# Optimization experiments

Hardware: AMD Instinct MI355X
Metric: run time of the kernel (lower is better)

## Reference

```python
import jax, jax.numpy as jnp
import numpy as np

D_MODEL = 1024
N_HEAD = 16
DEPTH = D_MODEL // N_HEAD
B, N = 2, 2048


def setup_inputs() -> dict:
    key = jax.random.key(0)
    ks = jax.random.split(key, 9)
    s = 1.0 / np.sqrt(D_MODEL)
    inp = {
        "input": jax.random.normal(ks[0], (B, N, D_MODEL), dtype=jnp.float32),
        # causal boolean mask; True = keep (module masks where mask is False)
        "mask": jnp.broadcast_to(jnp.tril(jnp.ones((N, N), dtype=bool)), (B, N, N)),
        "Wq": jax.random.uniform(ks[1], (D_MODEL, D_MODEL), jnp.float32, -s, s),
        "bq": jax.random.uniform(ks[2], (D_MODEL,), jnp.float32, -s, s),
        "Wk": jax.random.uniform(ks[3], (D_MODEL, D_MODEL), jnp.float32, -s, s),
        "bk": jax.random.uniform(ks[4], (D_MODEL,), jnp.float32, -s, s),
        "Wv": jax.random.uniform(ks[5], (D_MODEL, D_MODEL), jnp.float32, -s, s),
        "bv": jax.random.uniform(ks[6], (D_MODEL,), jnp.float32, -s, s),
        "Wo": jax.random.uniform(ks[7], (D_MODEL, D_MODEL), jnp.float32, -s, s),
        "bo": jax.random.uniform(ks[8], (D_MODEL,), jnp.float32, -s, s),
    }
    return inp


def reference(input, mask, Wq, bq, Wk, bk, Wv, bv, Wo, bo):
    b, n, _ = input.shape
    # projections (dropout in eval mode = identity)
    q = (input @ Wq.T + bq).reshape(b, n, N_HEAD, DEPTH)
    k = (input @ Wk.T + bk).reshape(b, n, N_HEAD, DEPTH)
    v = (input @ Wv.T + bv).reshape(b, n, N_HEAD, DEPTH)
    scale = 1.0 / np.sqrt(DEPTH)
    # scores: [b, h, q, k]
    scores = jnp.einsum("bqhd,bkhd->bhqk", q, k) * scale
    scores = jnp.where(mask[:, None, :, :], scores, -jnp.inf)
    attn = jax.nn.softmax(scores, axis=-1)
    out = jnp.einsum("bhqk,bkhd->bqhd", attn, v).reshape(b, n, D_MODEL)
    return out @ Wo.T + bo
```

## Files before the change

kernel.cpp:

```cpp
#include <hip/hip_runtime.h>
#include <stdint.h>

#define DM 1024
#define NH 16
#define DEPTH 64
#define BB 2
#define NN 2048
#define ROWS (BB*NN)

typedef __attribute__((ext_vector_type(8))) short short8;
typedef __attribute__((ext_vector_type(4))) short short4v;
typedef __attribute__((ext_vector_type(4))) float f32x4;

static __device__ __forceinline__ unsigned short f2b(float f) {
  unsigned u = __float_as_uint(f);
  u += 0x7fffu + ((u >> 16) & 1u);
  return (unsigned short)(u >> 16);
}

__global__ void cvt5_kernel(const float* __restrict__ s0, const float* __restrict__ s1,
                            const float* __restrict__ s2, const float* __restrict__ s3,
                            const float* __restrict__ s4,
                            unsigned short* __restrict__ d0, unsigned short* __restrict__ d1,
                            unsigned short* __restrict__ d2, unsigned short* __restrict__ d3,
                            unsigned short* __restrict__ d4) {
  const float* src; unsigned short* dst; int n4;
  const int seg = blockIdx.y;
  if (seg == 0)      { src = s0; dst = d0; n4 = ROWS * DM / 4; }
  else if (seg == 1) { src = s1; dst = d1; n4 = DM * DM / 4; }
  else if (seg == 2) { src = s2; dst = d2; n4 = DM * DM / 4; }
  else if (seg == 3) { src = s3; dst = d3; n4 = DM * DM / 4; }
  else               { src = s4; dst = d4; n4 = DM * DM / 4; }
  int i = blockIdx.x * blockDim.x + threadIdx.x;
  int stride = gridDim.x * blockDim.x;
  for (; i < n4; i += stride) {
    float4 v = reinterpret_cast<const float4*>(src)[i];
    short4v o;
    o.x = (short)f2b(v.x); o.y = (short)f2b(v.y);
    o.z = (short)f2b(v.z); o.w = (short)f2b(v.w);
    reinterpret_cast<short4v*>(dst)[i] = o;
  }
}

template<int OUTF32>
__global__ __launch_bounds__(256)
void gemm_bt(const unsigned short* __restrict__ A, const unsigned short* __restrict__ B,
             const float* __restrict__ bias0, const float* __restrict__ bias1,
             const float* __restrict__ bias2, float sc0,
             float* __restrict__ Cf, unsigned short* __restrict__ Cb,
             int K, int N) {
  __shared__ unsigned short As[128 * 32];
  __shared__ unsigned short Bs[128 * 32];
  const int tid = threadIdx.x;
  const int lane = tid & 63;
  const int w = tid >> 6;
  const int wr = w >> 1, wc = w & 1;
  const int l15 = lane & 15, l4 = lane >> 4;
  const int m0 = blockIdx.y * 128, n0 = blockIdx.x * 128;
  f32x4 acc[4][4] = {};
  const int nkt = K >> 5;
  for (int kt = 0; kt < nkt; ++kt) {
    const int kbase = kt * 32;
#pragma unroll
    for (int i = 0; i < 2; ++i) {
      int c = tid + i * 256;
      int row = c >> 2, ko = (c & 3) * 8;
      __builtin_amdgcn_global_load_lds(
          (__attribute__((address_space(1))) void*)(A + (size_t)(m0 + row) * K + kbase + ko),
          (__attribute__((address_space(3))) void*)((char*)As + c * 16), 16, 0, 0);
      __builtin_amdgcn_global_load_lds(
          (__attribute__((address_space(1))) void*)(B + (size_t)(n0 + row) * K + kbase + ko),
          (__attribute__((address_space(3))) void*)((char*)Bs + c * 16), 16, 0, 0);
    }
    __syncthreads();
    short8 a[4], b[4];
#pragma unroll
    for (int mi = 0; mi < 4; ++mi)
      a[mi] = *reinterpret_cast<const short8*>(&As[(wr * 64 + mi * 16 + l15) * 32 + l4 * 8]);
#pragma unroll
    for (int ni = 0; ni < 4; ++ni)
      b[ni] = *reinterpret_cast<const short8*>(&Bs[(wc * 64 + ni * 16 + l15) * 32 + l4 * 8]);
#pragma unroll
    for (int mi = 0; mi < 4; ++mi)
#pragma unroll
      for (int ni = 0; ni < 4; ++ni)
        acc[mi][ni] = __builtin_amdgcn_mfma_f32_16x16x32_bf16(a[mi], b[ni], acc[mi][ni], 0, 0, 0);
    __syncthreads();
  }
  const float* bp = bias0; int boff = 0;
  if (n0 >= 2048)      { bp = bias2; boff = 2048; }
  else if (n0 >= 1024) { bp = bias1; boff = 1024; }
  const float sc = (n0 < 1024) ? sc0 : 1.0f;
#pragma unroll
  for (int ni = 0; ni < 4; ++ni) {
    int col = n0 + wc * 64 + ni * 16 + l15;
    float bv = bp[col - boff];
#pragma unroll
    for (int mi = 0; mi < 4; ++mi) {
      f32x4 v = acc[mi][ni];
#pragma unroll
      for (int r = 0; r < 4; ++r) {
        int row = m0 + wr * 64 + mi * 16 + l4 * 4 + r;
        float outv = (v[r] + bv) * sc;
        if (OUTF32) Cf[(size_t)row * N + col] = outv;
        else        Cb[(size_t)row * N + col] = f2b(outv);
      }
    }
  }
}

__global__ __launch_bounds__(256)
void vtrans_kernel(const unsigned short* __restrict__ qkv, unsigned short* __restrict__ vt) {
  const int bh = blockIdx.y, b = bh >> 4, h = bh & 15;
  const int n0 = blockIdx.x * 64;
  __shared__ unsigned short t[64][72];
  const unsigned short* src = qkv + (size_t)(b * NN) * 3072 + 2048 + h * 64;
#pragma unroll
  for (int i = 0; i < 2; ++i) {
    int c = threadIdx.x + i * 256;
    int row = c >> 3, d0 = (c & 7) * 8;
    short8 v = *reinterpret_cast<const short8*>(src + (size_t)(n0 + row) * 3072 + d0);
#pragma unroll
    for (int j = 0; j < 8; ++j) t[d0 + j][row] = (unsigned short)v[j];
  }
  __syncthreads();
  unsigned short* dst = vt + ((size_t)(b * NH + h) * DEPTH) * NN + n0;
#pragma unroll
  for (int i = 0; i < 2; ++i) {
    int c = threadIdx.x + i * 256;
    int d = c >> 3, nn0 = (c & 7) * 8;
    short8 v;
#pragma unroll
    for (int j = 0; j < 8; ++j) v[j] = (short)t[d][nn0 + j];
    *reinterpret_cast<short8*>(dst + (size_t)d * NN + nn0) = v;
  }
}

__global__ __launch_bounds__(256)
void attn_kernel(const unsigned short* __restrict__ qkv, const unsigned short* __restrict__ vt,
                 unsigned short* __restrict__ aout) {
  const int tid = threadIdx.x, lane = tid & 63, w = tid >> 6;
  const int l15 = lane & 15, l4 = lane >> 4;
  const unsigned u = blockIdx.x * 4 + w;
  const int bh = u >> 6;
  const int ii = u & 63;
  const int b = bh >> 4, h = bh & 15;
  const unsigned short* Qp  = qkv + (size_t)(b * NN) * 3072 + h * 64;
  const unsigned short* Kp  = Qp + 1024;
  const unsigned short* Vtp = vt + (size_t)(b * NH + h) * DEPTH * NN;
  __shared__ unsigned short plds[4][16 * 40];
  unsigned short* pw = plds[w];

  for (int ip = 0; ip < 2; ++ip) {
    const int qt = ip ? (127 - ii) : ii;
    const int qp0 = qt * 16;
    const int nkt = (qt >> 1) + 1;
    short8 qf[2];
#pragma unroll
    for (int kk = 0; kk < 2; ++kk)
      qf[kk] = *reinterpret_cast<const short8*>(
          Qp + (size_t)(qp0 + l15) * 3072 + kk * 32 + l4 * 8);
    f32x4 o[4] = {};
    float m = -3.0e38f, l = 0.0f;
    short8 kf[2][2];
#pragma unroll
    for (int cf = 0; cf < 2; ++cf)
#pragma unroll
      for (int kk = 0; kk < 2; ++kk)
        kf[cf][kk] = *reinterpret_cast<const short8*>(
            Kp + (size_t)(cf * 16 + l15) * 3072 + kk * 32 + l4 * 8);

    for (int kt = 0; kt < nkt; ++kt) {
      const int k0 = kt * 32;
      f32x4 s[2];
#pragma unroll
      for (int cf = 0; cf < 2; ++cf) {
        f32x4 z = {};
        z = __builtin_amdgcn_mfma_f32_16x16x32_bf16(kf[cf][0], qf[0], z, 0, 0, 0);
        s[cf] = __builtin_amdgcn_mfma_f32_16x16x32_bf16(kf[cf][1], qf[1], z, 0, 0, 0);
      }
      short8 vf[4];
#pragma unroll
      for (int dn = 0; dn < 4; ++dn)
        vf[dn] = *reinterpret_cast<const short8*>(
            Vtp + (size_t)(dn * 16 + l15) * NN + k0 + l4 * 8);
      const int kn = (kt + 1 < nkt) ? k0 + 32 : k0;
#pragma unroll
      for (int cf = 0; cf < 2; ++cf)
#pragma unroll
        for (int kk = 0; kk < 2; ++kk)
          kf[cf][kk] = *reinterpret_cast<const short8*>(
              Kp + (size_t)(kn + cf * 16 + l15) * 3072 + kk * 32 + l4 * 8);
      float p[2][4];
      const bool diag = (kt == nkt - 1);
#pragma unroll
      for (int cf = 0; cf < 2; ++cf)
#pragma unroll
        for (int r = 0; r < 4; ++r) {
          float x = s[cf][r];
          if (diag && (k0 + cf * 16 + l4 * 4 + r > qp0 + l15)) x = -3.0e38f;
          p[cf][r] = x;
        }
      float pm = fmaxf(
          fmaxf(fmaxf(p[0][0], p[0][1]), fmaxf(p[0][2], p[0][3])),
          fmaxf(fmaxf(p[1][0], p[1][1]), fmaxf(p[1][2], p[1][3])));
      pm = fmaxf(pm, __shfl_xor(pm, 16));
      pm = fmaxf(pm, __shfl_xor(pm, 32));
      const float mn = fmaxf(m, pm);
      const float al = __expf(m - mn);
      m = mn;
      float ps = 0.0f;
#pragma unroll
      for (int cf = 0; cf < 2; ++cf)
#pragma unroll
        for (int r = 0; r < 4; ++r) {
          p[cf][r] = __expf(p[cf][r] - mn);
          ps += p[cf][r];
        }
      ps += __shfl_xor(ps, 16);
      ps += __shfl_xor(ps, 32);
      l = l * al + ps;
#pragma unroll
      for (int cf = 0; cf < 2; ++cf)
#pragma unroll
        for (int hh = 0; hh < 2; ++hh) {
          unsigned pk;
          asm("v_cvt_pk_bf16_f32 %0, %1, %2"
              : "=v"(pk) : "v"(p[cf][2 * hh]), "v"(p[cf][2 * hh + 1]));
          *reinterpret_cast<unsigned*>(&pw[l15 * 40 + cf * 16 + l4 * 4 + 2 * hh]) = pk;
        }
#pragma unroll
      for (int dn = 0; dn < 4; ++dn)
#pragma unroll
        for (int r = 0; r < 4; ++r) o[dn][r] *= al;
      short8 pf = *reinterpret_cast<const short8*>(&pw[l15 * 40 + l4 * 8]);
#pragma unroll
      for (int dn = 0; dn < 4; ++dn)
        o[dn] = __builtin_amdgcn_mfma_f32_16x16x32_bf16(vf[dn], pf, o[dn], 0, 0, 0);
    }
    const float inv = 1.0f / l;
    const int row = b * NN + qp0 + l15;
#pragma unroll
    for (int dn = 0; dn < 4; ++dn) {
      short4v ov;
#pragma unroll
      for (int r = 0; r < 4; ++r) ov[r] = (short)f2b(o[dn][r] * inv);
      *reinterpret_cast<short4v*>(&aout[(size_t)row * DM + h * 64 + dn * 16 + l4 * 4]) = ov;
    }
  }
}

extern "C" void kernel_launch(void* const* d_in, const int* in_sizes, int n_in,
                              void* d_out, int out_size, void* d_ws, size_t ws_size,
                              hipStream_t stream) {
  const float* X  = (const float*)d_in[0];
  const float* Wq = (const float*)d_in[2];
  const float* bq = (const float*)d_in[3];
  const float* Wk = (const float*)d_in[4];
  const float* bk = (const float*)d_in[5];
  const float* Wv = (const float*)d_in[6];
  const float* bv = (const float*)d_in[7];
  const float* Wo = (const float*)d_in[8];
  const float* bo = (const float*)d_in[9];
  float* out = (float*)d_out;

  char* ws = (char*)d_ws;
  unsigned short* Xb     = (unsigned short*)(ws);
  unsigned short* Wstack = (unsigned short*)(ws + 8ull  * 1024 * 1024);
  unsigned short* Wob    = (unsigned short*)(ws + 14ull * 1024 * 1024);
  unsigned short* QKV    = (unsigned short*)(ws + 16ull * 1024 * 1024);
  unsigned short* Vt     = (unsigned short*)(ws + 40ull * 1024 * 1024);
  unsigned short* AOut   = (unsigned short*)(ws + 48ull * 1024 * 1024);

  cvt5_kernel<<<dim3(128, 5), 256, 0, stream>>>(X, Wq, Wk, Wv, Wo,
                                                Xb, Wstack, Wstack + 1024 * 1024,
                                                Wstack + 2 * 1024 * 1024, Wob);

  gemm_bt<0><<<dim3(24, 32), 256, 0, stream>>>(Xb, Wstack, bq, bk, bv, 0.125f,
                                               nullptr, QKV, DM, 3072);
  vtrans_kernel<<<dim3(32, 32), 256, 0, stream>>>(QKV, Vt);
  attn_kernel<<<dim3(512), 256, 0, stream>>>(QKV, Vt, AOut);
  gemm_bt<1><<<dim3(8, 32), 256, 0, stream>>>(AOut, Wob, bo, bo, bo, 1.0f,
                                              out, nullptr, DM, DM);
}
```

Before: 305.7 us.

## Split attention KV range across wave pairs with LDS merge and lazy rescale

Each query tile's key range is now split between two waves, and their partial softmax states are merged through shared memory. The grid doubles and blocks are remapped so work is spread more evenly. The softmax switches to exp2 by folding log2(e) into the Q scale. It also skips the running-max rescale unless the new max exceeds the old by a threshold. This is meant to raise parallelism and cut per-tile latency and exp/rescale work. The cost is extra LDS traffic, two block-wide barriers per tile, and half of the waves sitting idle during the merge.

```diff
diff --git a/kernel.cpp b/kernel.cpp
--- a/kernel.cpp
+++ b/kernel.cpp
@@ -141,20 +141,29 @@
                  unsigned short* __restrict__ aout) {
   const int tid = threadIdx.x, lane = tid & 63, w = tid >> 6;
   const int l15 = lane & 15, l4 = lane >> 4;
-  const unsigned u = blockIdx.x * 4 + w;
-  const int bh = u >> 6;
-  const int ii = u & 63;
-  const int b = bh >> 4, h = bh & 15;
-  const unsigned short* Qp  = qkv + (size_t)(b * NN) * 3072 + h * 64;
+  const int blk = blockIdx.x;
+  const int g = (blk & 7) * 128 + (blk >> 3);
+  const int bh = g >> 5;
+  const int jj = g & 31;
+  const int pi = 2 * jj + (w >> 1);
+  const int half = w & 1;
+  const int batch = bh >> 4, h = bh & 15;
+  const unsigned short* Qp  = qkv + (size_t)(batch * NN) * 3072 + h * 64;
   const unsigned short* Kp  = Qp + 1024;
-  const unsigned short* Vtp = vt + (size_t)(b * NH + h) * DEPTH * NN;
+  const unsigned short* Vtp = vt + (size_t)(batch * NH + h) * DEPTH * NN;
   __shared__ unsigned short plds[4][16 * 40];
+  __shared__ float mergeO[4][16][68];
+  __shared__ float mergeM[4][16];
+  __shared__ float mergeL[4][16];
   unsigned short* pw = plds[w];
 
   for (int ip = 0; ip < 2; ++ip) {
-    const int qt = ip ? (127 - ii) : ii;
+    const int qt = ip ? (127 - pi) : pi;
     const int qp0 = qt * 16;
     const int nkt = (qt >> 1) + 1;
+    const int kmid = (nkt + 1) >> 1;
+    const int kb = half ? kmid : 0;
+    const int ke = half ? nkt : kmid;
     short8 qf[2];
 #pragma unroll
     for (int kk = 0; kk < 2; ++kk)
@@ -163,14 +172,16 @@
     f32x4 o[4] = {};
     float m = -3.0e38f, l = 0.0f;
     short8 kf[2][2];
-#pragma unroll
-    for (int cf = 0; cf < 2; ++cf)
-#pragma unroll
-      for (int kk = 0; kk < 2; ++kk)
-        kf[cf][kk] = *reinterpret_cast<const short8*>(
-            Kp + (size_t)(cf * 16 + l15) * 3072 + kk * 32 + l4 * 8);
-
-    for (int kt = 0; kt < nkt; ++kt) {
+    if (kb < ke) {
+#pragma unroll
+      for (int cf = 0; cf < 2; ++cf)
+#pragma unroll
+        for (int kk = 0; kk < 2; ++kk)
+          kf[cf][kk] = *reinterpret_cast<const short8*>(
+              Kp + (size_t)(kb * 32 + cf * 16 + l15) * 3072 + kk * 32 + l4 * 8);
+    }
+
+    for (int kt = kb; kt < ke; ++kt) {
       const int k0 = kt * 32;
       f32x4 s[2];
 #pragma unroll
@@ -184,7 +195,7 @@
       for (int dn = 0; dn < 4; ++dn)
         vf[dn] = *reinterpret_cast<const short8*>(
             Vtp + (size_t)(dn * 16 + l15) * NN + k0 + l4 * 8);
-      const int kn = (kt + 1 < nkt) ? k0 + 32 : k0;
+      const int kn = (kt + 1 < ke) ? k0 + 32 : k0;
 #pragma unroll
       for (int cf = 0; cf < 2; ++cf)
 #pragma unroll
@@ -206,20 +217,27 @@
           fmaxf(fmaxf(p[1][0], p[1][1]), fmaxf(p[1][2], p[1][3])));
       pm = fmaxf(pm, __shfl_xor(pm, 16));
       pm = fmaxf(pm, __shfl_xor(pm, 32));
-      const float mn = fmaxf(m, pm);
-      const float al = __expf(m - mn);
-      m = mn;
+      if (!__all(pm <= m + 11.5f)) {
+        const float mn = fmaxf(m, pm);
+        const float al = exp2f(m - mn);
+        m = mn;
+        l *= al;
+#pragma unroll
+        for (int dn = 0; dn < 4; ++dn)
+#pragma unroll
+          for (int r = 0; r < 4; ++r) o[dn][r] *= al;
+      }
       float ps = 0.0f;
 #pragma unroll
       for (int cf = 0; cf < 2; ++cf)
 #pragma unroll
         for (int r = 0; r < 4; ++r) {
-          p[cf][r] = __expf(p[cf][r] - mn);
+          p[cf][r] = exp2f(p[cf][r] - m);
           ps += p[cf][r];
         }
       ps += __shfl_xor(ps, 16);
       ps += __shfl_xor(ps, 32);
-      l = l * al + ps;
+      l += ps;
 #pragma unroll
       for (int cf = 0; cf < 2; ++cf)
 #pragma unroll
@@ -229,24 +247,35 @@
               : "=v"(pk) : "v"(p[cf][2 * hh]), "v"(p[cf][2 * hh + 1]));
           *reinterpret_cast<unsigned*>(&pw[l15 * 40 + cf * 16 + l4 * 4 + 2 * hh]) = pk;
         }
-#pragma unroll
-      for (int dn = 0; dn < 4; ++dn)
-#pragma unroll
-        for (int r = 0; r < 4; ++r) o[dn][r] *= al;
       short8 pf = *reinterpret_cast<const short8*>(&pw[l15 * 40 + l4 * 8]);
 #pragma unroll
       for (int dn = 0; dn < 4; ++dn)
         o[dn] = __builtin_amdgcn_mfma_f32_16x16x32_bf16(vf[dn], pf, o[dn], 0, 0, 0);
     }
-    const float inv = 1.0f / l;
-    const int row = b * NN + qp0 + l15;
-#pragma unroll
-    for (int dn = 0; dn < 4; ++dn) {
-      short4v ov;
-#pragma unroll
-      for (int r = 0; r < 4; ++r) ov[r] = (short)f2b(o[dn][r] * inv);
-      *reinterpret_cast<short4v*>(&aout[(size_t)row * DM + h * 64 + dn * 16 + l4 * 4]) = ov;
-    }
+    if (l4 == 0) { mergeM[w][l15] = m; mergeL[w][l15] = l; }
+#pragma unroll
+    for (int dn = 0; dn < 4; ++dn)
+      *reinterpret_cast<f32x4*>(&mergeO[w][l15][dn * 16 + l4 * 4]) = o[dn];
+    __syncthreads();
+    if (half == 0) {
+      const float m1 = mergeM[w ^ 1][l15];
+      const float l1 = mergeL[w ^ 1][l15];
+      const float mn = fmaxf(m, m1);
+      const float a0 = exp2f(m - mn);
+      const float a1 = exp2f(m1 - mn);
+      const float inv = 1.0f / (l * a0 + l1 * a1);
+      const int row = batch * NN + qp0 + l15;
+#pragma unroll
+      for (int dn = 0; dn < 4; ++dn) {
+        f32x4 o1 = *reinterpret_cast<const f32x4*>(&mergeO[w ^ 1][l15][dn * 16 + l4 * 4]);
+        short4v ov;
+#pragma unroll
+        for (int r = 0; r < 4; ++r)
+          ov[r] = (short)f2b((o[dn][r] * a0 + o1[r] * a1) * inv);
+        *reinterpret_cast<short4v*>(&aout[(size_t)row * DM + h * 64 + dn * 16 + l4 * 4]) = ov;
+      }
+    }
+    __syncthreads();
   }
 }
 
@@ -276,10 +305,10 @@
                                                 Xb, Wstack, Wstack + 1024 * 1024,
                                                 Wstack + 2 * 1024 * 1024, Wob);
 
-  gemm_bt<0><<<dim3(24, 32), 256, 0, stream>>>(Xb, Wstack, bq, bk, bv, 0.125f,
+  gemm_bt<0><<<dim3(24, 32), 256, 0, stream>>>(Xb, Wstack, bq, bk, bv, 0.18033688f,
                                                nullptr, QKV, DM, 3072);
   vtrans_kernel<<<dim3(32, 32), 256, 0, stream>>>(QKV, Vt);
-  attn_kernel<<<dim3(512), 256, 0, stream>>>(QKV, Vt, AOut);
+  attn_kernel<<<dim3(1024), 256, 0, stream>>>(QKV, Vt, AOut);
   gemm_bt<1><<<dim3(8, 32), 256, 0, stream>>>(AOut, Wob, bo, bo, bo, 1.0f,
                                               out, nullptr, DM, DM);
 }
```

Measured after the change: 310.7 us. Within noise of the previous version (+1.6%).
